# Kernel optimization log

Hardware: AMD Instinct MI355X
Metric: run time of the kernel (lower is better)

Reference implementation:

```python
import jax, jax.numpy as jnp
import numpy as np

SHAPES = ((80, 80), (40, 40), (20, 20), (10, 10))  # (H, W) per level
N_HEADS = 8
N_POINTS = 4
D_MODEL = 512  # double_d_model = 2*256 (densefusion=True)
D_FFN = 1024
B = 2
L = len(SHAPES)
S = sum(h * w for h, w in SHAPES)  # 8500
EPS = 1e-5


def _layernorm(x, g, b):
    m = jnp.mean(x, axis=-1, keepdims=True)
    v = jnp.mean((x - m) ** 2, axis=-1, keepdims=True)
    return (x - m) * jax.lax.rsqrt(v + EPS) * g + b


def _reference_points(shapes):
    # encoder get_reference_points with valid_ratios == 1 -> [S, 2] (x, y) in (0,1)
    refs = []
    for (H, W) in shapes:
        ry = (jnp.arange(H, dtype=jnp.float32) + 0.5) / H
        rx = (jnp.arange(W, dtype=jnp.float32) + 0.5) / W
        gy, gx = jnp.meshgrid(ry, rx, indexing='ij')
        refs.append(jnp.stack([gx.reshape(-1), gy.reshape(-1)], axis=-1))
    return jnp.concatenate(refs, axis=0)


def _sample_level(val, loc, H, W):
    # val: [B, H*W, h, d]; loc: [B, S, h, P, 2] normalized in [0,1]
    b, _, h, d = val.shape
    s, p = loc.shape[1], loc.shape[3]
    x = loc[..., 0] * W - 0.5
    y = loc[..., 1] * H - 0.5
    x0 = jnp.floor(x)
    y0 = jnp.floor(y)
    wx = x - x0
    wy = y - y0
    x0i = x0.astype(jnp.int32)
    y0i = y0.astype(jnp.int32)

    def gather(xi, yi):
        valid = ((xi >= 0) & (xi < W) & (yi >= 0) & (yi < H)).astype(val.dtype)
        idx = jnp.clip(yi, 0, H - 1) * W + jnp.clip(xi, 0, W - 1)  # [B,S,h,P]
        idx2 = jnp.transpose(idx, (0, 1, 3, 2)).reshape(b, s * p, h)  # [B,S*P,h]
        g = jnp.take_along_axis(val, idx2[..., None], axis=1)  # [B,S*P,h,d]
        vmask = jnp.transpose(valid, (0, 1, 3, 2))[..., None]  # [B,S,P,h,1]
        return g.reshape(b, s, p, h, d) * vmask

    v00 = gather(x0i, y0i)
    v01 = gather(x0i + 1, y0i)
    v10 = gather(x0i, y0i + 1)
    v11 = gather(x0i + 1, y0i + 1)
    wxT = jnp.transpose(wx, (0, 1, 3, 2))[..., None]
    wyT = jnp.transpose(wy, (0, 1, 3, 2))[..., None]
    return (v00 * (1 - wxT) * (1 - wyT) + v01 * wxT * (1 - wyT)
            + v10 * (1 - wxT) * wyT + v11 * wxT * wyT)  # [B,S,P,h,d]


def _forward(src, pos, w_off, b_off, w_attn, b_attn, w_val, b_val, w_out, b_out,
             ln1_g, ln1_b, w1, b1, w2, b2, ln2_g, ln2_b, shapes):
    b, s, c = src.shape
    h, p, l = N_HEADS, N_POINTS, len(shapes)
    d = c // h
    q = src + pos
    value = (src @ w_val + b_val).reshape(b, s, h, d)
    offsets = (q @ w_off + b_off).reshape(b, s, h, l, p, 2)
    attn = jax.nn.softmax((q @ w_attn + b_attn).reshape(b, s, h, l * p), axis=-1)
    attn = attn.reshape(b, s, h, l, p)
    ref = _reference_points(shapes)  # [S,2]
    # offset normalizer = (W_l, H_l)
    norm = jnp.array([[W, H] for (H, W) in shapes], dtype=src.dtype)  # [L,2]
    loc = ref[None, :, None, None, None, :] + offsets / norm[None, None, None, :, None, :]
    # split value per level and sample
    starts = np.cumsum([0] + [H * W for (H, W) in shapes])[:-1]
    sampled = []
    for lvl, (H, W) in enumerate(shapes):
        val_l = jax.lax.dynamic_slice_in_dim(value, int(starts[lvl]), H * W, axis=1)
        sampled.append(_sample_level(val_l, loc[:, :, :, lvl], H, W))
    sampled = jnp.stack(sampled)  # [L,B,S,P,h,d]
    out = jnp.einsum('lbqphd,bqhlp->bqhd', sampled, attn).reshape(b, s, c)
    attn_out = out @ w_out + b_out
    x = _layernorm(src + attn_out, ln1_g, ln1_b)
    ffn = jax.nn.relu(x @ w1 + b1) @ w2 + b2
    return _layernorm(x + ffn, ln2_g, ln2_b)


def setup_inputs() -> dict:
    key = jax.random.key(0)
    ks = jax.random.split(key, 20)
    sc = 0.02
    C = D_MODEL
    hLP = N_HEADS * L * N_POINTS
    f32 = jnp.float32
    inp = {
        'src': jax.random.normal(ks[0], (B, S, C), f32),
        'pos': jax.random.normal(ks[1], (B, S, C), f32),
        'w_off': jax.random.normal(ks[2], (C, hLP * 2), f32) * sc,
        'b_off': jax.random.normal(ks[3], (hLP * 2,), f32) * sc,
        'w_attn': jax.random.normal(ks[4], (C, hLP), f32) * sc,
        'b_attn': jax.random.normal(ks[5], (hLP,), f32) * sc,
        'w_val': jax.random.normal(ks[6], (C, C), f32) * sc,
        'b_val': jnp.zeros((C,), f32),
        'w_out': jax.random.normal(ks[7], (C, C), f32) * sc,
        'b_out': jnp.zeros((C,), f32),
        'ln1_g': jnp.ones((C,), f32),
        'ln1_b': jnp.zeros((C,), f32),
        'w1': jax.random.normal(ks[8], (C, D_FFN), f32) * sc,
        'b1': jnp.zeros((D_FFN,), f32),
        'w2': jax.random.normal(ks[9], (D_FFN, C), f32) * sc,
        'b2': jnp.zeros((C,), f32),
        'ln2_g': jnp.ones((C,), f32),
        'ln2_b': jnp.zeros((C,), f32),
        'spatial_shapes': jnp.array(SHAPES, dtype=jnp.int32),
    }
    return inp


def reference(src, pos, w_off, b_off, w_attn, b_attn, w_val, b_val, w_out, b_out,
              ln1_g, ln1_b, w1, b1, w2, b2, ln2_g, ln2_b, spatial_shapes):
    shapes = tuple((int(a), int(b)) for a, b in np.asarray(spatial_shapes))
    return _forward(src, pos, w_off, b_off, w_attn, b_attn, w_val, b_val, w_out, b_out,
                    ln1_g, ln1_b, w1, b1, w2, b2, ln2_g, ln2_b, shapes)
```

## Files before the change

kernel.cpp:

```cpp
#include <hip/hip_runtime.h>


typedef __bf16 bf16_t;
typedef __bf16 bf16x8 __attribute__((ext_vector_type(8)));
typedef __bf16 bf16x4 __attribute__((ext_vector_type(4)));
typedef float  f32x2  __attribute__((ext_vector_type(2)));
typedef float  f32x4  __attribute__((ext_vector_type(4)));
typedef float  f32x16 __attribute__((ext_vector_type(16)));

#define M_ROWS 17000
#define S_LEN  8500

__device__ inline void store_c(float* p, float v)  { *p = v; }
__device__ inline void store_c(bf16_t* p, float v) { *p = (bf16_t)v; }

__device__ inline float4 load4f(const float* p)  { return *(const float4*)p; }
__device__ inline float4 load4f(const bf16_t* p) {
    bf16x4 v = *(const bf16x4*)p;
    return make_float4((float)v[0], (float)v[1], (float)v[2], (float)v[3]);
}

__device__ inline void pk_fma(f32x2& a, f32x2 x, f32x2 y) {
    asm("v_pk_fma_f32 %0, %1, %2, %0" : "+v"(a) : "v"(x), "v"(y));
}

__device__ __forceinline__ void glds16(const bf16_t* g, bf16_t* l) {
    __builtin_amdgcn_global_load_lds(
        (const __attribute__((address_space(1))) void*)g,
        (__attribute__((address_space(3))) void*)l, 16, 0, 0);
}

__device__ inline int swz_flat() {
    int o   = blockIdx.x + gridDim.x * blockIdx.y;
    int nwg = gridDim.x * gridDim.y;
    int q = nwg >> 3, r = nwg & 7;
    int xcd = o & 7, s = o >> 3;
    return (xcd < r ? xcd * (q + 1) : r * (q + 1) + (xcd - r) * q) + s;
}

__global__ __launch_bounds__(256)
void prep_kernel(const float* __restrict__ w_val, const float* __restrict__ w_off,
                 const float* __restrict__ w_attn, const float* __restrict__ w_out,
                 const float* __restrict__ w1, const float* __restrict__ w2,
                 const float* __restrict__ b_off, const float* __restrict__ b_attn,
                 bf16_t* __restrict__ wt_val, bf16_t* __restrict__ wt_oa,
                 bf16_t* __restrict__ wt_out, bf16_t* __restrict__ wt_w1,
                 bf16_t* __restrict__ wt_w2, float* __restrict__ bias_oa) {
    int z = blockIdx.z;
    if (z == 6) {
        if (blockIdx.x == 0 && blockIdx.y == 0) {
            for (int i = threadIdx.x; i < 384; i += 256)
                bias_oa[i] = (i < 256) ? b_off[i] : b_attn[i - 256];
        }
        return;
    }
    const float* in; bf16_t* out; int K, N;
    switch (z) {
        case 0: in = w_val;  out = wt_val;                     K = 512;  N = 512;  break;
        case 1: in = w_off;  out = wt_oa;                      K = 512;  N = 256;  break;
        case 2: in = w_attn; out = wt_oa + (size_t)256 * 512;  K = 512;  N = 128;  break;
        case 3: in = w_out;  out = wt_out;                     K = 512;  N = 512;  break;
        case 4: in = w1;     out = wt_w1;                      K = 512;  N = 1024; break;
        default: in = w2;    out = wt_w2;                      K = 1024; N = 512;  break;
    }
    int k0 = blockIdx.x * 32, n0 = blockIdx.y * 32;
    if (k0 >= K || n0 >= N) return;
    __shared__ float s[32][33];
    int tx = threadIdx.x & 31, ty = threadIdx.x >> 5;
    #pragma unroll
    for (int i = 0; i < 4; i++)
        s[ty + 8 * i][tx] = in[(size_t)(k0 + ty + 8 * i) * N + n0 + tx];
    __syncthreads();
    #pragma unroll
    for (int i = 0; i < 4; i++)
        out[(size_t)(n0 + ty + 8 * i) * K + k0 + tx] = (bf16_t)s[tx][ty + 8 * i];
}

__global__ __launch_bounds__(256)
void add_q_kernel(const float* __restrict__ a, const float* __restrict__ b,
                  bf16_t* __restrict__ q, bf16_t* __restrict__ src_bf, int n4) {
    int i = blockIdx.x * 256 + threadIdx.x;
    if (i >= n4) return;
    float4 av = *(const float4*)(a + (size_t)i * 4);
    float4 bv = *(const float4*)(b + (size_t)i * 4);
    bf16x4 sv, ov;
    sv[0] = (bf16_t)av.x; sv[1] = (bf16_t)av.y; sv[2] = (bf16_t)av.z; sv[3] = (bf16_t)av.w;
    ov[0] = (bf16_t)(av.x + bv.x);
    ov[1] = (bf16_t)(av.y + bv.y);
    ov[2] = (bf16_t)(av.z + bv.z);
    ov[3] = (bf16_t)(av.w + bv.w);
    *(bf16x4*)(q      + (size_t)i * 4) = ov;
    *(bf16x4*)(src_bf + (size_t)i * 4) = sv;
}


#define GEMM_SETUP                                                                 \
    const int tid  = threadIdx.x;                                                  \
    const int wave = tid >> 6;                                                     \
    const int lane = tid & 63;                                                     \
    const int l31  = lane & 31;                                                    \
    const int pl   = lane >> 5;                                                    \
    const int kx   = (l31 >> 1) & 3;                                               \
    const int st_r = wave * 32 + (lane >> 2);                                      \
    const int st_c = ((lane & 3) ^ ((lane >> 3) & 3)) * 8;

#define GEMM128_CORE(A_PTR, WT_PTR, K_DIM, EPILOGUE)                               \
    GEMM_SETUP                                                                     \
    const int wr = (wave >> 1) * 64;                                               \
    const int wc = (wave & 1) * 64;                                                \
    const bf16_t* gsA0 = A_PTR  + (size_t)min(row0 + st_r,      M_ROWS - 1) * (K_DIM) + st_c; \
    const bf16_t* gsA1 = A_PTR  + (size_t)min(row0 + st_r + 16, M_ROWS - 1) * (K_DIM) + st_c; \
    const bf16_t* gsB0 = WT_PTR + (size_t)(col0 + st_r) * (K_DIM) + st_c;          \
    const bf16_t* gsB1 = WT_PTR + (size_t)(col0 + st_r + 16) * (K_DIM) + st_c;     \
    f32x16 acc[2][2];                                                              \
    _Pragma("unroll")                                                              \
    for (int i = 0; i < 2; i++)                                                    \
        _Pragma("unroll")                                                          \
        for (int j = 0; j < 2; j++)                                                \
            _Pragma("unroll")                                                      \
            for (int r = 0; r < 16; r++) acc[i][j][r] = 0.f;                       \
    glds16(gsA0, &As[0][wave * 32][0]);                                            \
    glds16(gsA1, &As[0][wave * 32 + 16][0]);                                       \
    glds16(gsB0, &Bs[0][wave * 32][0]);                                            \
    glds16(gsB1, &Bs[0][wave * 32 + 16][0]);                                       \
    const int nIter = (K_DIM) >> 5;                                                \
    for (int it = 0; it < nIter; it++) {                                           \
        const int cur = it & 1;                                                    \
        __syncthreads();                                                           \
        if (it + 1 < nIter) {                                                      \
            const int ko = (it + 1) << 5;                                          \
            glds16(gsA0 + ko, &As[cur ^ 1][wave * 32][0]);                         \
            glds16(gsA1 + ko, &As[cur ^ 1][wave * 32 + 16][0]);                    \
            glds16(gsB0 + ko, &Bs[cur ^ 1][wave * 32][0]);                         \
            glds16(gsB1 + ko, &Bs[cur ^ 1][wave * 32 + 16][0]);                    \
        }                                                                          \
        const char* Ab = (const char*)&As[cur][0][0];                              \
        const char* Bb = (const char*)&Bs[cur][0][0];                              \
        _Pragma("unroll")                                                          \
        for (int kh = 0; kh < 2; kh++) {                                           \
            const int sA = ((kh * 2 + pl) ^ kx) << 4;                              \
            bf16x8 a0 = *(const bf16x8*)(Ab + ((wr      + l31) << 6) + sA);        \
            bf16x8 a1 = *(const bf16x8*)(Ab + ((wr + 32 + l31) << 6) + sA);        \
            bf16x8 b0 = *(const bf16x8*)(Bb + ((wc      + l31) << 6) + sA);        \
            bf16x8 b1 = *(const bf16x8*)(Bb + ((wc + 32 + l31) << 6) + sA);        \
            acc[0][0] = __builtin_amdgcn_mfma_f32_32x32x16_bf16(a0, b0, acc[0][0], 0, 0, 0); \
            acc[0][1] = __builtin_amdgcn_mfma_f32_32x32x16_bf16(a0, b1, acc[0][1], 0, 0, 0); \
            acc[1][0] = __builtin_amdgcn_mfma_f32_32x32x16_bf16(a1, b0, acc[1][0], 0, 0, 0); \
            acc[1][1] = __builtin_amdgcn_mfma_f32_32x32x16_bf16(a1, b1, acc[1][1], 0, 0, 0); \
        }                                                                          \
    }                                                                              \
    EPILOGUE

#define GEMM64_CORE(A_PTR, WT_PTR, K_DIM, EPILOGUE)                                \
    GEMM_SETUP                                                                     \
    const int wr    = wave * 32;                                                   \
    const int st_rB = wave * 16 + (lane >> 2);                                     \
    const bf16_t* gsA0 = A_PTR  + (size_t)min(row0 + st_r,      M_ROWS - 1) * (K_DIM) + st_c; \
    const bf16_t* gsA1 = A_PTR  + (size_t)min(row0 + st_r + 16, M_ROWS - 1) * (K_DIM) + st_c; \
    const bf16_t* gsB0 = WT_PTR + (size_t)(col0 + st_rB) * (K_DIM) + st_c;         \
    f32x16 acc[2];                                                                 \
    _Pragma("unroll")                                                              \
    for (int j = 0; j < 2; j++)                                                    \
        _Pragma("unroll")                                                          \
        for (int r = 0; r < 16; r++) acc[j][r] = 0.f;                              \
    glds16(gsA0, &As[0][wave * 32][0]);                                            \
    glds16(gsA1, &As[0][wave * 32 + 16][0]);                                       \
    glds16(gsB0, &Bs[0][wave * 16][0]);                                            \
    const int nIter = (K_DIM) >> 5;                                                \
    for (int it = 0; it < nIter; it++) {                                           \
        const int cur = it & 1;                                                    \
        __syncthreads();                                                           \
        if (it + 1 < nIter) {                                                      \
            const int ko = (it + 1) << 5;                                          \
            glds16(gsA0 + ko, &As[cur ^ 1][wave * 32][0]);                         \
            glds16(gsA1 + ko, &As[cur ^ 1][wave * 32 + 16][0]);                    \
            glds16(gsB0 + ko, &Bs[cur ^ 1][wave * 16][0]);                         \
        }                                                                          \
        const char* Ab = (const char*)&As[cur][0][0];                              \
        const char* Bb = (const char*)&Bs[cur][0][0];                              \
        _Pragma("unroll")                                                          \
        for (int kh = 0; kh < 2; kh++) {                                           \
            const int sA = ((kh * 2 + pl) ^ kx) << 4;                              \
            bf16x8 a0 = *(const bf16x8*)(Ab + ((wr + l31) << 6) + sA);             \
            bf16x8 b0 = *(const bf16x8*)(Bb + ((     l31) << 6) + sA);             \
            bf16x8 b1 = *(const bf16x8*)(Bb + ((32 + l31) << 6) + sA);             \
            acc[0] = __builtin_amdgcn_mfma_f32_32x32x16_bf16(a0, b0, acc[0], 0, 0, 0); \
            acc[1] = __builtin_amdgcn_mfma_f32_32x32x16_bf16(a0, b1, acc[1], 0, 0, 0); \
        }                                                                          \
    }                                                                              \
    EPILOGUE

template<typename OT, bool RELU, int KD>
__global__ __launch_bounds__(256)
void gemm128_kernel(const bf16_t* __restrict__ A, const bf16_t* __restrict__ Wt,
                    const float* __restrict__ bias, OT* __restrict__ Cout, int N) {
    __shared__ bf16_t As[2][128][32];
    __shared__ bf16_t Bs[2][128][32];
    const int wg = swz_flat();
    const int NY = gridDim.y;
    const int row0 = (wg / NY) * 128;
    const int col0 = (wg % NY) * 128;
    GEMM128_CORE(A, Wt, KD,
        {
            _Pragma("unroll")
            for (int i = 0; i < 2; i++)
                _Pragma("unroll")
                for (int j = 0; j < 2; j++) {
                    int col = col0 + wc + j * 32 + l31;
                    float bcol = bias[col];
                    _Pragma("unroll")
                    for (int reg = 0; reg < 16; reg++) {
                        int row = row0 + wr + i * 32 + (reg & 3) + 8 * (reg >> 2) + 4 * (lane >> 5);
                        if (row < M_ROWS) {
                            float v = acc[i][j][reg] + bcol;
                            if (RELU) v = fmaxf(v, 0.f);
                            store_c(Cout + (size_t)row * N + col, v);
                        }
                    }
                }
        }
    )
}

template<typename OT, bool RELU, int KD>
__global__ __launch_bounds__(256)
void gemm64_kernel(const bf16_t* __restrict__ A, const bf16_t* __restrict__ Wt,
                   const float* __restrict__ bias, OT* __restrict__ Cout, int N) {
    __shared__ bf16_t As[2][128][32];
    __shared__ bf16_t Bs[2][64][32];
    const int wg = swz_flat();
    const int NY = gridDim.y;
    const int row0 = (wg / NY) * 128;
    const int col0 = (wg % NY) * 64;
    GEMM64_CORE(A, Wt, KD,
        {
            _Pragma("unroll")
            for (int j = 0; j < 2; j++) {
                int col = col0 + j * 32 + l31;
                float bcol = bias[col];
                _Pragma("unroll")
                for (int reg = 0; reg < 16; reg++) {
                    int row = row0 + wr + (reg & 3) + 8 * (reg >> 2) + 4 * (lane >> 5);
                    if (row < M_ROWS) {
                        float v = acc[j][reg] + bcol;
                        if (RELU) v = fmaxf(v, 0.f);
                        store_c(Cout + (size_t)row * N + col, v);
                    }
                }
            }
        }
    )
}

__global__ __launch_bounds__(256)
void gemm_voa_kernel(const bf16_t* __restrict__ src_bf, const bf16_t* __restrict__ q,
                     const bf16_t* __restrict__ wt_val, const bf16_t* __restrict__ wt_oa,
                     const float* __restrict__ b_val, const float* __restrict__ bias_oa,
                     bf16_t* __restrict__ value, float* __restrict__ oa) {
    __shared__ bf16_t As[2][128][32];
    __shared__ bf16_t Bs[2][64][32];
    const int wg = swz_flat();
    const int by = wg % 14;
    const bool isV  = by < 8;
    const int col0  = (isV ? by : by - 8) * 64;
    const int row0  = (wg / 14) * 128;
    const bf16_t* Ap  = isV ? src_bf : q;
    const bf16_t* Wp  = isV ? wt_val : wt_oa;
    const float* bp   = isV ? b_val : bias_oa;
    GEMM64_CORE(Ap, Wp, 512,
        {
            _Pragma("unroll")
            for (int j = 0; j < 2; j++) {
                int col = col0 + j * 32 + l31;
                float bcol = bp[col];
                _Pragma("unroll")
                for (int reg = 0; reg < 16; reg++) {
                    int row = row0 + wr + (reg & 3) + 8 * (reg >> 2) + 4 * (lane >> 5);
                    if (row < M_ROWS) {
                        float v = acc[j][reg] + bcol;
                        if (isV) value[(size_t)row * 512 + col] = (bf16_t)v;
                        else     oa[(size_t)row * 384 + col] = v;
                    }
                }
            }
        }
    )
}

__global__ __launch_bounds__(256)
void sample_kernel(const bf16_t* __restrict__ value, const float* __restrict__ oa,
                   bf16_t* __restrict__ out) {
    __shared__ __align__(16) int sAW[4][2][8][68];
    const int wave = threadIdx.x >> 6;
    const int lane = threadIdx.x & 63;
    const int h    = lane >> 3;
    const int sub  = lane & 7;
    const int bs   = swz_flat() * 4 + wave;
    const int b    = bs / S_LEN;
    const int s    = bs - b * S_LEN;

    float rx, ry;
    if (s < 6400)      { int i = s;        const float inv = 1.f/80.f; ry = ((i/80) + 0.5f)*inv; rx = ((i%80) + 0.5f)*inv; }
    else if (s < 8000) { int i = s - 6400; const float inv = 1.f/40.f; ry = ((i/40) + 0.5f)*inv; rx = ((i%40) + 0.5f)*inv; }
    else if (s < 8400) { int i = s - 8000; const float inv = 1.f/20.f; ry = ((i/20) + 0.5f)*inv; rx = ((i%20) + 0.5f)*inv; }
    else               { int i = s - 8400; const float inv = 1.f/10.f; ry = ((i/10) + 0.5f)*inv; rx = ((i%10) + 0.5f)*inv; }

    const int WH[4]  = {80, 40, 20, 10};
    const int LST[4] = {0, 6400, 8000, 8400};
    const int ll = sub >> 1;
    const int W  = WH[ll];
    const int LS = LST[ll];

    const float* row = oa + (size_t)bs * 384;
    float4 o4 = *(const float4*)(row + h * 32 + sub * 4);
    float2 lg = *(const float2*)(row + 256 + h * 16 + sub * 2);

    float mx = fmaxf(lg.x, lg.y);
    mx = fmaxf(mx, __shfl_xor(mx, 1, 64));
    mx = fmaxf(mx, __shfl_xor(mx, 2, 64));
    mx = fmaxf(mx, __shfl_xor(mx, 4, 64));
    float e0 = __expf(lg.x - mx), e1 = __expf(lg.y - mx);
    float sm = e0 + e1;
    sm += __shfl_xor(sm, 1, 64);
    sm += __shfl_xor(sm, 2, 64);
    sm += __shfl_xor(sm, 4, 64);
    float pinv = 1.f / sm;

    #pragma unroll
    for (int t = 0; t < 2; t++) {
        float ox = t ? o4.z : o4.x;
        float oy = t ? o4.w : o4.y;
        float p  = (t ? e1 : e0) * pinv;
        float x = fmaf(rx, (float)W, ox) - 0.5f;
        float y = fmaf(ry, (float)W, oy) - 0.5f;
        float fx = floorf(x), fy = floorf(y);
        float wx = x - fx, wy = y - fy;
        int ix = (int)fx, iy = (int)fy;
        #pragma unroll
        for (int k2 = 0; k2 < 4; k2++) {
            int cx = ix + (k2 & 1);
            int cy = iy + (k2 >> 1);
            float wgt = p * ((k2 & 1) ? wx : 1.f - wx) * ((k2 >> 1) ? wy : 1.f - wy);
            if (cx < 0 || cx >= W || cy < 0 || cy >= W) wgt = 0.f;
            int xc = min(max(cx, 0), W - 1);
            int yc = min(max(cy, 0), W - 1);
            int c = sub * 8 + t * 4 + k2;
            sAW[wave][0][h][c] = LS + yc * W + xc;
            sAW[wave][1][h][c] = __float_as_int(wgt);
        }
    }
    __syncthreads();

    const bf16_t* vb = value + ((size_t)b * S_LEN) * 512 + h * 64 + sub * 8;
    f32x2 a01 = {0.f, 0.f}, a23 = {0.f, 0.f}, a45 = {0.f, 0.f}, a67 = {0.f, 0.f};

    #define ACC8(V, WW) {                                                          \
        f32x2 ws; ws[0] = (WW); ws[1] = (WW);                                      \
        f32x2 pv;                                                                  \
        pv[0] = __uint_as_float((V).x << 16);                                      \
        pv[1] = __uint_as_float((V).x & 0xffff0000u); pk_fma(a01, pv, ws);         \
        pv[0] = __uint_as_float((V).y << 16);                                      \
        pv[1] = __uint_as_float((V).y & 0xffff0000u); pk_fma(a23, pv, ws);         \
        pv[0] = __uint_as_float((V).z << 16);                                      \
        pv[1] = __uint_as_float((V).z & 0xffff0000u); pk_fma(a45, pv, ws);         \
        pv[0] = __uint_as_float((V).w << 16);                                      \
        pv[1] = __uint_as_float((V).w & 0xffff0000u); pk_fma(a67, pv, ws); }

    #pragma unroll 2
    for (int c8 = 0; c8 < 64; c8 += 8) {
        int4   ia = *(const int4*)  &sAW[wave][0][h][c8];
        int4   ib = *(const int4*)  &sAW[wave][0][h][c8 + 4];
        float4 wa = *(const float4*)&sAW[wave][1][h][c8];
        float4 wb = *(const float4*)&sAW[wave][1][h][c8 + 4];
        uint4 v0 = *(const uint4*)(vb + (size_t)ia.x * 512);
        uint4 v1 = *(const uint4*)(vb + (size_t)ia.y * 512);
        uint4 v2 = *(const uint4*)(vb + (size_t)ia.z * 512);
        uint4 v3 = *(const uint4*)(vb + (size_t)ia.w * 512);
        uint4 v4 = *(const uint4*)(vb + (size_t)ib.x * 512);
        uint4 v5 = *(const uint4*)(vb + (size_t)ib.y * 512);
        uint4 v6 = *(const uint4*)(vb + (size_t)ib.z * 512);
        uint4 v7 = *(const uint4*)(vb + (size_t)ib.w * 512);
        ACC8(v0, wa.x) ACC8(v1, wa.y) ACC8(v2, wa.z) ACC8(v3, wa.w)
        ACC8(v4, wb.x) ACC8(v5, wb.y) ACC8(v6, wb.z) ACC8(v7, wb.w)
    }
    #undef ACC8

    bf16x8 ov;
    ov[0] = (bf16_t)a01[0]; ov[1] = (bf16_t)a01[1];
    ov[2] = (bf16_t)a23[0]; ov[3] = (bf16_t)a23[1];
    ov[4] = (bf16_t)a45[0]; ov[5] = (bf16_t)a45[1];
    ov[6] = (bf16_t)a67[0]; ov[7] = (bf16_t)a67[1];
    *(bf16x8*)(out + (size_t)bs * 512 + h * 64 + sub * 8) = ov;
}

template<typename INA, typename INB, typename OT>
__global__ __launch_bounds__(256)
void ln_kernel(const INA* __restrict__ Xa, const INB* __restrict__ Xb,
               const float* __restrict__ g, const float* __restrict__ be,
               OT* __restrict__ out, int M) {
    int wave = threadIdx.x >> 6;
    int lane = threadIdx.x & 63;
    int row = blockIdx.x * 4 + wave;
    if (row >= M) return;
    size_t base = (size_t)row * 512;
    float v[8];
    float s = 0.f, sq = 0.f;
    #pragma unroll
    for (int p = 0; p < 2; p++) {
        int idx = p * 256 + lane * 4;
        float4 a4 = load4f(Xa + base + idx);
        float4 b4 = load4f(Xb + base + idx);
        float t0 = a4.x + b4.x, t1 = a4.y + b4.y, t2 = a4.z + b4.z, t3 = a4.w + b4.w;
        v[p*4+0] = t0; v[p*4+1] = t1; v[p*4+2] = t2; v[p*4+3] = t3;
        s  += t0 + t1 + t2 + t3;
        sq += t0*t0 + t1*t1 + t2*t2 + t3*t3;
    }
    #pragma unroll
    for (int off = 32; off > 0; off >>= 1) {
        s  += __shfl_xor(s, off, 64);
        sq += __shfl_xor(sq, off, 64);
    }
    float mean = s * (1.f / 512.f);
    float var  = sq * (1.f / 512.f) - mean * mean;
    float rstd = rsqrtf(var + 1e-5f);
    #pragma unroll
    for (int p = 0; p < 2; p++) {
        int idx = p * 256 + lane * 4;
        #pragma unroll
        for (int j = 0; j < 4; j++) {
            int col = idx + j;
            float o = (v[p*4+j] - mean) * rstd * g[col] + be[col];
            store_c(out + base + col, o);
        }
    }
}

extern "C" void kernel_launch(void* const* d_in, const int* in_sizes, int n_in,
                              void* d_out, int out_size, void* d_ws, size_t ws_size,
                              hipStream_t stream) {
    const float* src    = (const float*)d_in[0];
    const float* pos    = (const float*)d_in[1];
    const float* w_off  = (const float*)d_in[2];
    const float* b_off  = (const float*)d_in[3];
    const float* w_attn = (const float*)d_in[4];
    const float* b_attn = (const float*)d_in[5];
    const float* w_val  = (const float*)d_in[6];
    const float* b_val  = (const float*)d_in[7];
    const float* w_out  = (const float*)d_in[8];
    const float* b_out  = (const float*)d_in[9];
    const float* ln1_g  = (const float*)d_in[10];
    const float* ln1_b  = (const float*)d_in[11];
    const float* w1     = (const float*)d_in[12];
    const float* b1     = (const float*)d_in[13];
    const float* w2     = (const float*)d_in[14];
    const float* b2     = (const float*)d_in[15];
    const float* ln2_g  = (const float*)d_in[16];
    const float* ln2_b  = (const float*)d_in[17];

    const int M = M_ROWS;
    char* ws = (char*)d_ws;
    size_t o = 0;
    auto alloc = [&](size_t bytes) { size_t r = o; o += (bytes + 255) & ~(size_t)255; return r; };

    size_t off_q       = alloc((size_t)M * 512 * 2);
    size_t off_srcbf   = alloc((size_t)M * 512 * 2);
    size_t off_value   = alloc((size_t)M * 512 * 2);
    size_t off_sampled = alloc((size_t)M * 512 * 2);
    size_t off_oa      = alloc((size_t)M * 384 * 4);
    size_t off_attnout = alloc((size_t)M * 512 * 2);
    size_t off_x       = alloc((size_t)M * 512 * 2);
    size_t off_wtval   = alloc((size_t)512 * 512 * 2);
    size_t off_wtoa    = alloc((size_t)384 * 512 * 2);
    size_t off_wtout   = alloc((size_t)512 * 512 * 2);
    size_t off_wtw1    = alloc((size_t)1024 * 512 * 2);
    size_t off_wtw2    = alloc((size_t)512 * 1024 * 2);
    size_t off_boa     = alloc((size_t)384 * 4);

    bf16_t* q        = (bf16_t*)(ws + off_q);
    bf16_t* src_bf   = (bf16_t*)(ws + off_srcbf);
    bf16_t* value    = (bf16_t*)(ws + off_value);
    bf16_t* sampled  = (bf16_t*)(ws + off_sampled);
    float*  oa       = (float*)(ws + off_oa);
    bf16_t* attn_out = (bf16_t*)(ws + off_attnout);
    bf16_t* x        = (bf16_t*)(ws + off_x);
    bf16_t* hidden   = (bf16_t*)(ws + off_sampled);
    bf16_t* ffn_out  = (bf16_t*)(ws + off_attnout);
    bf16_t* wt_val   = (bf16_t*)(ws + off_wtval);
    bf16_t* wt_oa    = (bf16_t*)(ws + off_wtoa);
    bf16_t* wt_out   = (bf16_t*)(ws + off_wtout);
    bf16_t* wt_w1    = (bf16_t*)(ws + off_wtw1);
    bf16_t* wt_w2    = (bf16_t*)(ws + off_wtw2);
    float*  bias_oa  = (float*)(ws + off_boa);
    float*  outp     = (float*)d_out;

    prep_kernel<<<dim3(32, 32, 7), 256, 0, stream>>>(
        w_val, w_off, w_attn, w_out, w1, w2, b_off, b_attn,
        wt_val, wt_oa, wt_out, wt_w1, wt_w2, bias_oa);

    add_q_kernel<<<(M * 512 / 4 + 255) / 256, 256, 0, stream>>>(src, pos, q, src_bf, M * 512 / 4);

    const int MT = (M + 127) / 128;

    gemm_voa_kernel<<<dim3(MT, 14), 256, 0, stream>>>(src_bf, q, wt_val, wt_oa, b_val, bias_oa, value, oa);

    sample_kernel<<<M / 4, 256, 0, stream>>>(value, oa, sampled);

    gemm64_kernel<bf16_t, false, 512><<<dim3(MT, 8), 256, 0, stream>>>(sampled, wt_out, b_out, attn_out, 512);

    ln_kernel<float, bf16_t, bf16_t><<<(M + 3) / 4, 256, 0, stream>>>(src, attn_out, ln1_g, ln1_b, x, M);

    gemm128_kernel<bf16_t, true, 512><<<dim3(MT, 8), 256, 0, stream>>>(x, wt_w1, b1, hidden, 1024);
    gemm64_kernel<bf16_t, false, 1024><<<dim3(MT, 8), 256, 0, stream>>>(hidden, wt_w2, b2, ffn_out, 512);

    ln_kernel<bf16_t, bf16_t, float><<<(M + 3) / 4, 256, 0, stream>>>(x, ffn_out, ln2_g, ln2_b, outp, M);
}
```

Before: 350.5 us.

## Use triple-buffered LDS pipeline with partial vmcnt waits in GEMM cores

Both GEMM cores move from double to triple buffering in shared memory. They prefetch two K-tiles ahead and replace __syncthreads with a barrier that waits only until the older stage's global-to-LDS loads have landed. The aim is to hide global load latency behind more MFMA work per barrier. The cost is 50% more LDS per block, which may lower occupancy.

```diff
diff --git a/kernel.cpp b/kernel.cpp
--- a/kernel.cpp
+++ b/kernel.cpp
@@ -103,6 +103,34 @@
     const int kx   = (l31 >> 1) & 3;                                               \
     const int st_r = wave * 32 + (lane >> 2);                                      \
     const int st_c = ((lane & 3) ^ ((lane >> 3) & 3)) * 8;
+
+#define BAR_CNT(Nw)                                                                \
+    asm volatile("s_waitcnt vmcnt(" #Nw ") lgkmcnt(0)" ::: "memory");              \
+    __builtin_amdgcn_sched_barrier(0);                                             \
+    __builtin_amdgcn_s_barrier();                                                  \
+    __builtin_amdgcn_sched_barrier(0);
+
+#define STAGE128(S, KO)                                                            \
+    glds16(gsA0 + (KO), &As[S][wave * 32][0]);                                     \
+    glds16(gsA1 + (KO), &As[S][wave * 32 + 16][0]);                                \
+    glds16(gsB0 + (KO), &Bs[S][wave * 32][0]);                                     \
+    glds16(gsB1 + (KO), &Bs[S][wave * 32 + 16][0]);
+
+#define MFMA128(S) {                                                               \
+    const char* Ab = (const char*)&As[S][0][0];                                    \
+    const char* Bb = (const char*)&Bs[S][0][0];                                    \
+    _Pragma("unroll")                                                              \
+    for (int kh = 0; kh < 2; kh++) {                                               \
+        const int sA = ((kh * 2 + pl) ^ kx) << 4;                                  \
+        bf16x8 a0 = *(const bf16x8*)(Ab + ((wr      + l31) << 6) + sA);            \
+        bf16x8 a1 = *(const bf16x8*)(Ab + ((wr + 32 + l31) << 6) + sA);            \
+        bf16x8 b0 = *(const bf16x8*)(Bb + ((wc      + l31) << 6) + sA);            \
+        bf16x8 b1 = *(const bf16x8*)(Bb + ((wc + 32 + l31) << 6) + sA);            \
+        acc[0][0] = __builtin_amdgcn_mfma_f32_32x32x16_bf16(a0, b0, acc[0][0], 0, 0, 0); \
+        acc[0][1] = __builtin_amdgcn_mfma_f32_32x32x16_bf16(a0, b1, acc[0][1], 0, 0, 0); \
+        acc[1][0] = __builtin_amdgcn_mfma_f32_32x32x16_bf16(a1, b0, acc[1][0], 0, 0, 0); \
+        acc[1][1] = __builtin_amdgcn_mfma_f32_32x32x16_bf16(a1, b1, acc[1][1], 0, 0, 0); \
+    } }
 
 #define GEMM128_CORE(A_PTR, WT_PTR, K_DIM, EPILOGUE)                               \
     GEMM_SETUP                                                                     \
@@ -119,37 +147,41 @@
         for (int j = 0; j < 2; j++)                                                \
             _Pragma("unroll")                                                      \
             for (int r = 0; r < 16; r++) acc[i][j][r] = 0.f;                       \
-    glds16(gsA0, &As[0][wave * 32][0]);                                            \
-    glds16(gsA1, &As[0][wave * 32 + 16][0]);                                       \
-    glds16(gsB0, &Bs[0][wave * 32][0]);                                            \
-    glds16(gsB1, &Bs[0][wave * 32 + 16][0]);                                       \
+    STAGE128(0, 0)                                                                 \
+    STAGE128(1, 32)                                                                \
     const int nIter = (K_DIM) >> 5;                                                \
-    for (int it = 0; it < nIter; it++) {                                           \
-        const int cur = it & 1;                                                    \
-        __syncthreads();                                                           \
-        if (it + 1 < nIter) {                                                      \
-            const int ko = (it + 1) << 5;                                          \
-            glds16(gsA0 + ko, &As[cur ^ 1][wave * 32][0]);                         \
-            glds16(gsA1 + ko, &As[cur ^ 1][wave * 32 + 16][0]);                    \
-            glds16(gsB0 + ko, &Bs[cur ^ 1][wave * 32][0]);                         \
-            glds16(gsB1 + ko, &Bs[cur ^ 1][wave * 32 + 16][0]);                    \
+    int cs = 0;                                                                    \
+    for (int it = 0; it < nIter - 1; it++) {                                       \
+        BAR_CNT(4)                                                                 \
+        if (it + 2 < nIter) {                                                      \
+            int s2 = cs + 2; if (s2 >= 3) s2 -= 3;                                 \
+            const int ko = (it + 2) << 5;                                          \
+            STAGE128(s2, ko)                                                       \
         }                                                                          \
-        const char* Ab = (const char*)&As[cur][0][0];                              \
-        const char* Bb = (const char*)&Bs[cur][0][0];                              \
-        _Pragma("unroll")                                                          \
-        for (int kh = 0; kh < 2; kh++) {                                           \
-            const int sA = ((kh * 2 + pl) ^ kx) << 4;                              \
-            bf16x8 a0 = *(const bf16x8*)(Ab + ((wr      + l31) << 6) + sA);        \
-            bf16x8 a1 = *(const bf16x8*)(Ab + ((wr + 32 + l31) << 6) + sA);        \
-            bf16x8 b0 = *(const bf16x8*)(Bb + ((wc      + l31) << 6) + sA);        \
-            bf16x8 b1 = *(const bf16x8*)(Bb + ((wc + 32 + l31) << 6) + sA);        \
-            acc[0][0] = __builtin_amdgcn_mfma_f32_32x32x16_bf16(a0, b0, acc[0][0], 0, 0, 0); \
-            acc[0][1] = __builtin_amdgcn_mfma_f32_32x32x16_bf16(a0, b1, acc[0][1], 0, 0, 0); \
-            acc[1][0] = __builtin_amdgcn_mfma_f32_32x32x16_bf16(a1, b0, acc[1][0], 0, 0, 0); \
-            acc[1][1] = __builtin_amdgcn_mfma_f32_32x32x16_bf16(a1, b1, acc[1][1], 0, 0, 0); \
-        }                                                                          \
+        MFMA128(cs)                                                                \
+        cs++; if (cs == 3) cs = 0;                                                 \
     }                                                                              \
+    BAR_CNT(0)                                                                     \
+    MFMA128(cs)                                                                    \
     EPILOGUE
+
+#define STAGE64(S, KO)                                                             \
+    glds16(gsA0 + (KO), &As[S][wave * 32][0]);                                     \
+    glds16(gsA1 + (KO), &As[S][wave * 32 + 16][0]);                                \
+    glds16(gsB0 + (KO), &Bs[S][wave * 16][0]);
+
+#define MFMA64(S) {                                                                \
+    const char* Ab = (const char*)&As[S][0][0];                                    \
+    const char* Bb = (const char*)&Bs[S][0][0];                                    \
+    _Pragma("unroll")                                                              \
+    for (int kh = 0; kh < 2; kh++) {                                               \
+        const int sA = ((kh * 2 + pl) ^ kx) << 4;                                  \
+        bf16x8 a0 = *(const bf16x8*)(Ab + ((wr + l31) << 6) + sA);                 \
+        bf16x8 b0 = *(const bf16x8*)(Bb + ((     l31) << 6) + sA);                 \
+        bf16x8 b1 = *(const bf16x8*)(Bb + ((32 + l31) << 6) + sA);                 \
+        acc[0] = __builtin_amdgcn_mfma_f32_32x32x16_bf16(a0, b0, acc[0], 0, 0, 0); \
+        acc[1] = __builtin_amdgcn_mfma_f32_32x32x16_bf16(a0, b1, acc[1], 0, 0, 0); \
+    } }
 
 #define GEMM64_CORE(A_PTR, WT_PTR, K_DIM, EPILOGUE)                                \
     GEMM_SETUP                                                                     \
@@ -163,39 +195,30 @@
     for (int j = 0; j < 2; j++)                                                    \
         _Pragma("unroll")                                                          \
         for (int r = 0; r < 16; r++) acc[j][r] = 0.f;                              \
-    glds16(gsA0, &As[0][wave * 32][0]);                                            \
-    glds16(gsA1, &As[0][wave * 32 + 16][0]);                                       \
-    glds16(gsB0, &Bs[0][wave * 16][0]);                                            \
+    STAGE64(0, 0)                                                                  \
+    STAGE64(1, 32)                                                                 \
     const int nIter = (K_DIM) >> 5;                                                \
-    for (int it = 0; it < nIter; it++) {                                           \
-        const int cur = it & 1;                                                    \
-        __syncthreads();                                                           \
-        if (it + 1 < nIter) {                                                      \
-            const int ko = (it + 1) << 5;                                          \
-            glds16(gsA0 + ko, &As[cur ^ 1][wave * 32][0]);                         \
-            glds16(gsA1 + ko, &As[cur ^ 1][wave * 32 + 16][0]);                    \
-            glds16(gsB0 + ko, &Bs[cur ^ 1][wave * 16][0]);                         \
+    int cs = 0;                                                                    \
+    for (int it = 0; it < nIter - 1; it++) {                                       \
+        BAR_CNT(3)                                                                 \
+        if (it + 2 < nIter) {                                                      \
+            int s2 = cs + 2; if (s2 >= 3) s2 -= 3;                                 \
+            const int ko = (it + 2) << 5;                                          \
+            STAGE64(s2, ko)                                                        \
         }                                                                          \
-        const char* Ab = (const char*)&As[cur][0][0];                              \
-        const char* Bb = (const char*)&Bs[cur][0][0];                              \
-        _Pragma("unroll")                                                          \
-        for (int kh = 0; kh < 2; kh++) {                                           \
-            const int sA = ((kh * 2 + pl) ^ kx) << 4;                              \
-            bf16x8 a0 = *(const bf16x8*)(Ab + ((wr + l31) << 6) + sA);             \
-            bf16x8 b0 = *(const bf16x8*)(Bb + ((     l31) << 6) + sA);             \
-            bf16x8 b1 = *(const bf16x8*)(Bb + ((32 + l31) << 6) + sA);             \
-            acc[0] = __builtin_amdgcn_mfma_f32_32x32x16_bf16(a0, b0, acc[0], 0, 0, 0); \
-            acc[1] = __builtin_amdgcn_mfma_f32_32x32x16_bf16(a0, b1, acc[1], 0, 0, 0); \
-        }                                                                          \
+        MFMA64(cs)                                                                 \
+        cs++; if (cs == 3) cs = 0;                                                 \
     }                                                                              \
+    BAR_CNT(0)                                                                     \
+    MFMA64(cs)                                                                     \
     EPILOGUE
 
 template<typename OT, bool RELU, int KD>
 __global__ __launch_bounds__(256)
 void gemm128_kernel(const bf16_t* __restrict__ A, const bf16_t* __restrict__ Wt,
                     const float* __restrict__ bias, OT* __restrict__ Cout, int N) {
-    __shared__ bf16_t As[2][128][32];
-    __shared__ bf16_t Bs[2][128][32];
+    __shared__ bf16_t As[3][128][32];
+    __shared__ bf16_t Bs[3][128][32];
     const int wg = swz_flat();
     const int NY = gridDim.y;
     const int row0 = (wg / NY) * 128;
@@ -226,8 +249,8 @@
 __global__ __launch_bounds__(256)
 void gemm64_kernel(const bf16_t* __restrict__ A, const bf16_t* __restrict__ Wt,
                    const float* __restrict__ bias, OT* __restrict__ Cout, int N) {
-    __shared__ bf16_t As[2][128][32];
-    __shared__ bf16_t Bs[2][64][32];
+    __shared__ bf16_t As[3][128][32];
+    __shared__ bf16_t Bs[3][64][32];
     const int wg = swz_flat();
     const int NY = gridDim.y;
     const int row0 = (wg / NY) * 128;
@@ -257,8 +280,8 @@
                      const bf16_t* __restrict__ wt_val, const bf16_t* __restrict__ wt_oa,
                      const float* __restrict__ b_val, const float* __restrict__ bias_oa,
                      bf16_t* __restrict__ value, float* __restrict__ oa) {
-    __shared__ bf16_t As[2][128][32];
-    __shared__ bf16_t Bs[2][64][32];
+    __shared__ bf16_t As[3][128][32];
+    __shared__ bf16_t Bs[3][64][32];
     const int wg = swz_flat();
     const int by = wg % 14;
     const bool isV  = by < 8;
```

New measurement: 370.3 us. +5.7%, slower.
